# Optimization experiments

Hardware: AMD Instinct MI355X
Metric: run time of the kernel (lower is better)

Reference implementation:

```python
import jax, jax.numpy as jnp
import numpy as np

N_NODES = 20000
N_EDGES = 320000
H = 128
IN = 256  # num_hidden + num_in
SCALE = 30.0
EPS = 1e-5


def _ln(x, g, b):
    m = jnp.mean(x, axis=-1, keepdims=True)
    v = jnp.var(x, axis=-1, keepdims=True)
    return (x - m) * jax.lax.rsqrt(v + EPS) * g + b


def setup_inputs() -> dict:
    key = jax.random.key(0)
    ks = jax.random.split(key, 16)
    s_in = 1.0 / np.sqrt(IN)
    s_h = 1.0 / np.sqrt(H)
    s_4h = 1.0 / np.sqrt(4 * H)
    return {
        "h_V": jax.random.normal(ks[0], (N_NODES, H), jnp.float32),
        "h_E": jax.random.normal(ks[1], (N_EDGES, IN), jnp.float32),
        "edge_idx": jax.random.randint(ks[2], (2, N_EDGES), 0, N_NODES, jnp.int32),
        # weights stored (in, out): y = x @ W + b (equivalent to torch Linear)
        "W1_w": jax.random.uniform(ks[3], (IN, H), jnp.float32, -s_in, s_in),
        "W1_b": jax.random.uniform(ks[4], (H,), jnp.float32, -s_in, s_in),
        "W2_w": jax.random.uniform(ks[5], (H, H), jnp.float32, -s_h, s_h),
        "W2_b": jax.random.uniform(ks[6], (H,), jnp.float32, -s_h, s_h),
        "W3_w": jax.random.uniform(ks[7], (H, H), jnp.float32, -s_h, s_h),
        "W3_b": jax.random.uniform(ks[8], (H,), jnp.float32, -s_h, s_h),
        "n1_g": jnp.ones((H,), jnp.float32),
        "n1_b": jnp.zeros((H,), jnp.float32),
        "d1_w": jax.random.uniform(ks[9], (H, 4 * H), jnp.float32, -s_h, s_h),
        "d1_b": jax.random.uniform(ks[10], (4 * H,), jnp.float32, -s_h, s_h),
        "d2_w": jax.random.uniform(ks[11], (4 * H, H), jnp.float32, -s_4h, s_4h),
        "d2_b": jax.random.uniform(ks[12], (H,), jnp.float32, -s_4h, s_4h),
        "n2_g": jnp.ones((H,), jnp.float32),
        "n2_b": jnp.zeros((H,), jnp.float32),
    }


def reference(h_V, h_E, edge_idx, W1_w, W1_b, W2_w, W2_b, W3_w, W3_b,
              n1_g, n1_b, d1_w, d1_b, d2_w, d2_b, n2_g, n2_b):
    gelu = lambda x: jax.nn.gelu(x, approximate=False)  # torch F.gelu default = erf
    src_idx = edge_idx[0]
    # edge MLP: W3(gelu(W2(gelu(W1(h_E)))))
    h_message = gelu(h_E @ W1_w + W1_b)
    h_message = gelu(h_message @ W2_w + W2_b)
    h_message = h_message @ W3_w + W3_b
    # scatter_sum over source node, then scale
    dh = jax.ops.segment_sum(h_message, src_idx, num_segments=N_NODES) / SCALE
    h_V = _ln(h_V + dh, n1_g, n1_b)  # dropout is identity at eval
    dh = gelu(h_V @ d1_w + d1_b) @ d2_w + d2_b
    h_V = _ln(h_V + dh, n2_g, n2_b)
    return h_V
```

## Files before the change

### kernel.cpp

```cpp
#include <hip/hip_runtime.h>
#include <hip/hip_bf16.h>
#include <math.h>

#define NNODES 20000
#define NEDGES 320000
#define HDIM   128
#define INDIM  256
#define INV_SCALE (1.0f/30.0f)
#define LN_EPS 1e-5f

typedef __bf16 bf16x8 __attribute__((ext_vector_type(8)));
typedef float  f32x4  __attribute__((ext_vector_type(4)));
typedef _Float16 half4_t __attribute__((ext_vector_type(4)));
typedef _Float16 half8_t __attribute__((ext_vector_type(8)));
typedef unsigned short ushort_t;

__device__ __forceinline__ unsigned short f2bf(float f) {
    union { __hip_bfloat16 h; unsigned short u; } c;
    c.h = __float2bfloat16(f);
    return c.u;
}

__device__ __forceinline__ float gelu_fast(float x) {
    const float z = x * (1.595769122f + 0.071354816f * x * x);
    return x / (1.0f + __expf(-z));
}

__device__ __forceinline__ f32x4 mfma_bf16(bf16x8 a, bf16x8 b, f32x4 c) {
    return __builtin_amdgcn_mfma_f32_16x16x32_bf16(a, b, c, 0, 0, 0);
}

#define CVT8(dst, v0, v1) { union { bf16x8 v; ushort_t u[8]; } c_; \
    c_.u[0] = f2bf((v0).x); c_.u[1] = f2bf((v0).y); c_.u[2] = f2bf((v0).z); c_.u[3] = f2bf((v0).w); \
    c_.u[4] = f2bf((v1).x); c_.u[5] = f2bf((v1).y); c_.u[6] = f2bf((v1).z); c_.u[7] = f2bf((v1).w); \
    (dst) = c_.v; }

__global__ void prep_all(const float* __restrict__ W1, const float* __restrict__ W2,
                         const float* __restrict__ W3, ushort_t* __restrict__ WswE,
                         const float* __restrict__ D1, const float* __restrict__ D2,
                         ushort_t* __restrict__ D1sw, ushort_t* __restrict__ D2sw,
                         const int* __restrict__ src, int* __restrict__ cnt) {
    const int id = blockIdx.x * 256 + threadIdx.x;
    if (id < 65536) {
        const float* W; int base, idx; bool perm = false;
        if (id < 32768)      { W = W1; base = 0;     idx = id; }
        else if (id < 49152) { W = W2; base = 32768; idx = id - 32768; }
        else                 { W = W3; base = 49152; idx = id - 49152; perm = true; }
        const int j = idx & 7, lane = (idx >> 3) & 63, t = (idx >> 9) & 7, s = idx >> 12;
        const int k = s * 32 + (lane >> 4) * 8 + j;
        const int n = perm ? (2 * ((t >> 1) * 16 + (lane & 15)) + (t & 1))
                           : (t * 16 + (lane & 15));
        WswE[base + idx] = f2bf(W[k * HDIM + n]);
    } else if (id < 196608) {
        const int nid = id - 65536;
        if (nid < 65536) {
            const int idx = nid;
            const int j = idx & 7, lane = (idx >> 3) & 63, f = idx >> 9;
            const int t = f & 31, s = f >> 5;
            const int k = s * 32 + (lane >> 4) * 8 + j;
            const int n = t * 16 + (lane & 15);
            D1sw[idx] = f2bf(D1[k * 512 + n]);
        } else {
            const int idx = nid - 65536;
            const int j = idx & 7, lane = (idx >> 3) & 63, f = idx >> 9;
            const int t = f & 7, s = f >> 3;
            const int k = s * 32 + (lane >> 4) * 8 + j;
            const int n = t * 16 + (lane & 15);
            D2sw[idx] = f2bf(D2[k * HDIM + n]);
        }
    } else {
        const int e = id - 196608;
        if (e < NEDGES) atomicAdd(&cnt[src[e]], 1);
    }
}

__launch_bounds__(1024)
__global__ void scan_counts(const int* __restrict__ cnt,
                            int* __restrict__ off, int* __restrict__ off2) {
    __shared__ int tot[1024];
    const int t = threadIdx.x;
    const int base = t * 20;
    int local[20]; int s = 0;
    #pragma unroll
    for (int i = 0; i < 20; ++i) {
        const int v = (base + i < NNODES) ? cnt[base + i] : 0;
        local[i] = s; s += v;
    }
    tot[t] = s;
    __syncthreads();
    for (int d = 1; d < 1024; d <<= 1) {
        const int v = (t >= d) ? tot[t - d] : 0;
        __syncthreads();
        tot[t] += v;
        __syncthreads();
    }
    const int excl = (t == 0) ? 0 : tot[t - 1];
    #pragma unroll
    for (int i = 0; i < 20; ++i)
        if (base + i < NNODES) { off[base + i] = excl + local[i]; off2[base + i] = excl + local[i]; }
    if (t == 1023) off[NNODES] = NEDGES;
}

__global__ void fill_perm(const int* __restrict__ src, int* __restrict__ off2,
                          int* __restrict__ perm) {
    const int e = blockIdx.x * 256 + threadIdx.x;
    if (e < NEDGES) {
        const int p = atomicAdd(&off2[src[e]], 1);
        perm[p] = e;
    }
}

#define A1S 272
#define SY  136

__launch_bounds__(256, 3)
__global__ void edge_mlp_v2(const float* __restrict__ hE,
                            const ushort_t* __restrict__ Wsw,
                            const float* __restrict__ b1,
                            const float* __restrict__ b2,
                            const float* __restrict__ b3,
                            _Float16* __restrict__ msg) {
    __shared__ __align__(16) ushort_t A1[64 * A1S];
    __shared__ __align__(16) ushort_t A2[64 * SY];

    const int tid = threadIdx.x;
    const int wave = tid >> 6, lane = tid & 63;
    const int quad = lane >> 4, l16 = lane & 15;
    const size_t e0 = (size_t)blockIdx.x * 64;
    const int T0 = wave * 2;

    {
        const int row = tid >> 2, q = tid & 3;
        const float4* src = (const float4*)(hE + (e0 + row) * INDIM + q * 64);
        ushort_t* dst = A1 + row * A1S + q * 64;
        #pragma unroll
        for (int i = 0; i < 8; ++i) {
            const float4 v0 = src[2 * i], v1 = src[2 * i + 1];
            bf16x8 a; CVT8(a, v0, v1);
            *(bf16x8*)(dst + i * 8) = a;
        }
    }

    f32x4 acc[4][2];
    bf16x8 bcur[2], bnxt[2];

    #pragma unroll
    for (int t = 0; t < 2; ++t) {
        const float bv = b1[(T0 + t) * 16 + l16];
        #pragma unroll
        for (int rt = 0; rt < 4; ++rt) acc[rt][t] = (f32x4){bv, bv, bv, bv};
    }
    bcur[0] = *(const bf16x8*)(Wsw + (size_t)((0 * 8 + T0 + 0) * 64 + lane) * 8);
    bcur[1] = *(const bf16x8*)(Wsw + (size_t)((0 * 8 + T0 + 1) * 64 + lane) * 8);
    __syncthreads();
    #pragma unroll
    for (int s = 0; s < 8; ++s) {
        if (s < 7) {
            bnxt[0] = *(const bf16x8*)(Wsw + (size_t)(((s + 1) * 8 + T0 + 0) * 64 + lane) * 8);
            bnxt[1] = *(const bf16x8*)(Wsw + (size_t)(((s + 1) * 8 + T0 + 1) * 64 + lane) * 8);
        }
        bf16x8 a[4];
        #pragma unroll
        for (int rt = 0; rt < 4; ++rt)
            a[rt] = *(const bf16x8*)(A1 + (rt * 16 + l16) * A1S + s * 32 + quad * 8);
        #pragma unroll
        for (int rt = 0; rt < 4; ++rt) {
            acc[rt][0] = mfma_bf16(a[rt], bcur[0], acc[rt][0]);
            acc[rt][1] = mfma_bf16(a[rt], bcur[1], acc[rt][1]);
        }
        bcur[0] = bnxt[0]; bcur[1] = bnxt[1];
    }
    #pragma unroll
    for (int rt = 0; rt < 4; ++rt)
        #pragma unroll
        for (int t = 0; t < 2; ++t)
            #pragma unroll
            for (int r = 0; r < 4; ++r)
                A2[(rt * 16 + quad * 4 + r) * SY + (T0 + t) * 16 + l16] =
                    f2bf(gelu_fast(acc[rt][t][r]));
    __syncthreads();

    #pragma unroll
    for (int t = 0; t < 2; ++t) {
        const float bv = b2[(T0 + t) * 16 + l16];
        #pragma unroll
        for (int rt = 0; rt < 4; ++rt) acc[rt][t] = (f32x4){bv, bv, bv, bv};
    }
    bcur[0] = *(const bf16x8*)(Wsw + 32768 + (size_t)((0 * 8 + T0 + 0) * 64 + lane) * 8);
    bcur[1] = *(const bf16x8*)(Wsw + 32768 + (size_t)((0 * 8 + T0 + 1) * 64 + lane) * 8);
    #pragma unroll
    for (int s = 0; s < 4; ++s) {
        if (s < 3) {
            bnxt[0] = *(const bf16x8*)(Wsw + 32768 + (size_t)(((s + 1) * 8 + T0 + 0) * 64 + lane) * 8);
            bnxt[1] = *(const bf16x8*)(Wsw + 32768 + (size_t)(((s + 1) * 8 + T0 + 1) * 64 + lane) * 8);
        }
        bf16x8 a[4];
        #pragma unroll
        for (int rt = 0; rt < 4; ++rt)
            a[rt] = *(const bf16x8*)(A2 + (rt * 16 + l16) * SY + s * 32 + quad * 8);
        #pragma unroll
        for (int rt = 0; rt < 4; ++rt) {
            acc[rt][0] = mfma_bf16(a[rt], bcur[0], acc[rt][0]);
            acc[rt][1] = mfma_bf16(a[rt], bcur[1], acc[rt][1]);
        }
        bcur[0] = bnxt[0]; bcur[1] = bnxt[1];
    }
    __syncthreads();
    #pragma unroll
    for (int rt = 0; rt < 4; ++rt)
        #pragma unroll
        for (int t = 0; t < 2; ++t)
            #pragma unroll
            for (int r = 0; r < 4; ++r)
                A2[(rt * 16 + quad * 4 + r) * SY + (T0 + t) * 16 + l16] =
                    f2bf(gelu_fast(acc[rt][t][r]));
    __syncthreads();

    #pragma unroll
    for (int t = 0; t < 2; ++t) {
        const float bv = b3[2 * (wave * 16 + l16) + t];
        #pragma unroll
        for (int rt = 0; rt < 4; ++rt) acc[rt][t] = (f32x4){bv, bv, bv, bv};
    }
    bcur[0] = *(const bf16x8*)(Wsw + 49152 + (size_t)((0 * 8 + T0 + 0) * 64 + lane) * 8);
    bcur[1] = *(const bf16x8*)(Wsw + 49152 + (size_t)((0 * 8 + T0 + 1) * 64 + lane) * 8);
    #pragma unroll
    for (int s = 0; s < 4; ++s) {
        if (s < 3) {
            bnxt[0] = *(const bf16x8*)(Wsw + 49152 + (size_t)(((s + 1) * 8 + T0 + 0) * 64 + lane) * 8);
            bnxt[1] = *(const bf16x8*)(Wsw + 49152 + (size_t)(((s + 1) * 8 + T0 + 1) * 64 + lane) * 8);
        }
        bf16x8 a[4];
        #pragma unroll
        for (int rt = 0; rt < 4; ++rt)
            a[rt] = *(const bf16x8*)(A2 + (rt * 16 + l16) * SY + s * 32 + quad * 8);
        #pragma unroll
        for (int rt = 0; rt < 4; ++rt) {
            acc[rt][0] = mfma_bf16(a[rt], bcur[0], acc[rt][0]);
            acc[rt][1] = mfma_bf16(a[rt], bcur[1], acc[rt][1]);
        }
        bcur[0] = bnxt[0]; bcur[1] = bnxt[1];
    }

    #pragma unroll
    for (int rt = 0; rt < 4; ++rt)
        #pragma unroll
        for (int r = 0; r < 4; ++r) {
            const size_t row = e0 + rt * 16 + quad * 4 + r;
            union { _Float16 h[2]; unsigned int u; } pk;
            pk.h[0] = (_Float16)acc[rt][0][r];
            pk.h[1] = (_Float16)acc[rt][1][r];
            ((unsigned int*)(msg + row * HDIM))[wave * 16 + l16] = pk.u;
        }
}

__launch_bounds__(256)
__global__ void gather_sum(const _Float16* __restrict__ msg,
                           const int* __restrict__ perm,
                           const int* __restrict__ off,
                           const float* __restrict__ hV,
                           float* __restrict__ xout) {
    const int tid = threadIdx.x;
    const int slot = tid >> 5, l32 = tid & 31;
    const int node = blockIdx.x * 8 + slot;
    const int j0 = off[node], j1 = off[node + 1];
    float a0 = 0.f, a1 = 0.f, a2 = 0.f, a3 = 0.f;
    int j = j0;
    for (; j + 1 < j1; j += 2) {
        const int ea = perm[j], eb = perm[j + 1];
        const half4_t ma = *(const half4_t*)(msg + (size_t)ea * HDIM + l32 * 4);
        const half4_t mb = *(const half4_t*)(msg + (size_t)eb * HDIM + l32 * 4);
        a0 += (float)ma[0] + (float)mb[0];
        a1 += (float)ma[1] + (float)mb[1];
        a2 += (float)ma[2] + (float)mb[2];
        a3 += (float)ma[3] + (float)mb[3];
    }
    if (j < j1) {
        const int ea = perm[j];
        const half4_t ma = *(const half4_t*)(msg + (size_t)ea * HDIM + l32 * 4);
        a0 += (float)ma[0]; a1 += (float)ma[1]; a2 += (float)ma[2]; a3 += (float)ma[3];
    }
    const float4 hv = *(const float4*)(hV + (size_t)node * HDIM + l32 * 4);
    const float4 o = {hv.x + a0 * INV_SCALE, hv.y + a1 * INV_SCALE,
                      hv.z + a2 * INV_SCALE, hv.w + a3 * INV_SCALE};
    *(float4*)(xout + (size_t)node * HDIM + l32 * 4) = o;
}

__launch_bounds__(256)
__global__ void node_mfma_x(const float* __restrict__ xin,
                            const float* __restrict__ n1g, const float* __restrict__ n1b,
                            const ushort_t* __restrict__ D1sw, const float* __restrict__ D1b,
                            const ushort_t* __restrict__ D2sw, const float* __restrict__ D2b,
                            const float* __restrict__ n2g, const float* __restrict__ n2b,
                            float* __restrict__ out) {
    __shared__ __align__(16) float xs[32 * HDIM];
    __shared__ __align__(16) ushort_t h1a[32 * SY];
    __shared__ __align__(16) ushort_t ua[32 * 520];
    __shared__ float mu_s[32], rs_s[32];

    const int tid = threadIdx.x;
    const int wave = tid >> 6, lane = tid & 63;
    const int quad = lane >> 4, l16 = lane & 15;
    const int n0 = blockIdx.x * 32;

    #pragma unroll
    for (int it = 0; it < 4; ++it) {
        const int f4 = it * 256 + tid;
        ((float4*)xs)[f4] = ((const float4*)(xin + (size_t)n0 * HDIM))[f4];
    }
    __syncthreads();

    {
        const int row = tid >> 3, q = tid & 7;
        float s = 0.f, s2 = 0.f;
        #pragma unroll
        for (int c = 0; c < 16; ++c) { const float v = xs[row * HDIM + q * 16 + c]; s += v; s2 += v * v; }
        #pragma unroll
        for (int o = 1; o < 8; o <<= 1) { s += __shfl_xor(s, o); s2 += __shfl_xor(s2, o); }
        if (q == 0) {
            const float m = s * (1.0f / HDIM);
            mu_s[row] = m;
            rs_s[row] = rsqrtf(s2 * (1.0f / HDIM) - m * m + LN_EPS);
        }
    }
    __syncthreads();

    #pragma unroll
    for (int it = 0; it < 2; ++it) {
        const int g = it * 256 + tid;
        const int row = g >> 4, col = (g & 15) * 8;
        const float mu = mu_s[row], rs = rs_s[row];
        union { bf16x8 v; ushort_t u[8]; } c;
        #pragma unroll
        for (int jj = 0; jj < 8; ++jj) {
            const float h1 = (xs[row * HDIM + col + jj] - mu) * rs * n1g[col + jj] + n1b[col + jj];
            c.u[jj] = f2bf(h1);
        }
        *(bf16x8*)(h1a + row * SY + col) = c.v;
    }
    __syncthreads();

    {
        f32x4 acc1[2][8];
        #pragma unroll
        for (int t = 0; t < 8; ++t) {
            const float bv = D1b[wave * 128 + t * 16 + l16];
            acc1[0][t] = (f32x4){bv, bv, bv, bv};
            acc1[1][t] = acc1[0][t];
        }
        #pragma unroll
        for (int s = 0; s < 4; ++s) {
            bf16x8 a[2];
            #pragma unroll
            for (int rt = 0; rt < 2; ++rt)
                a[rt] = *(const bf16x8*)(h1a + (rt * 16 + l16) * SY + s * 32 + quad * 8);
            #pragma unroll
            for (int t = 0; t < 8; ++t) {
                const bf16x8 b = *(const bf16x8*)(D1sw + (size_t)((s * 32 + wave * 8 + t) * 64 + lane) * 8);
                acc1[0][t] = mfma_bf16(a[0], b, acc1[0][t]);
                acc1[1][t] = mfma_bf16(a[1], b, acc1[1][t]);
            }
        }
        #pragma unroll
        for (int rt = 0; rt < 2; ++rt)
            #pragma unroll
            for (int t = 0; t < 8; ++t)
                #pragma unroll
                for (int r = 0; r < 4; ++r)
                    ua[(rt * 16 + quad * 4 + r) * 520 + wave * 128 + t * 16 + l16] =
                        f2bf(gelu_fast(acc1[rt][t][r]));
    }
    __syncthreads();

    f32x4 acc2[2][2];
    acc2[0][0] = (f32x4){0,0,0,0}; acc2[0][1] = acc2[0][0];
    acc2[1][0] = acc2[0][0];       acc2[1][1] = acc2[0][0];
    #pragma unroll
    for (int s = 0; s < 16; ++s) {
        bf16x8 a[2];
        #pragma unroll
        for (int rt = 0; rt < 2; ++rt)
            a[rt] = *(const bf16x8*)(ua + (rt * 16 + l16) * 520 + s * 32 + quad * 8);
        #pragma unroll
        for (int tt = 0; tt < 2; ++tt) {
            const bf16x8 b = *(const bf16x8*)(D2sw + (size_t)((s * 8 + wave * 2 + tt) * 64 + lane) * 8);
            acc2[0][tt] = mfma_bf16(a[0], b, acc2[0][tt]);
            acc2[1][tt] = mfma_bf16(a[1], b, acc2[1][tt]);
        }
    }
    __syncthreads();

    float* yf = (float*)ua;
    #pragma unroll
    for (int rt = 0; rt < 2; ++rt)
        #pragma unroll
        for (int tt = 0; tt < 2; ++tt)
            #pragma unroll
            for (int r = 0; r < 4; ++r) {
                const int row = rt * 16 + quad * 4 + r;
                const int col = wave * 32 + tt * 16 + l16;
                const float h1 = (xs[row * HDIM + col] - mu_s[row]) * rs_s[row] * n1g[col] + n1b[col];
                yf[row * HDIM + col] = h1 + acc2[rt][tt][r] + D2b[col];
            }
    __syncthreads();

    {
        const int row = tid >> 3, q = tid & 7;
        float s = 0.f, s2 = 0.f;
        #pragma unroll
        for (int c = 0; c < 16; ++c) { const float v = yf[row * HDIM + q * 16 + c]; s += v; s2 += v * v; }
        #pragma unroll
        for (int o = 1; o < 8; o <<= 1) { s += __shfl_xor(s, o); s2 += __shfl_xor(s2, o); }
        if (q == 0) {
            const float m = s * (1.0f / HDIM);
            mu_s[row] = m;
            rs_s[row] = rsqrtf(s2 * (1.0f / HDIM) - m * m + LN_EPS);
        }
    }
    __syncthreads();

    #pragma unroll
    for (int it = 0; it < 4; ++it) {
        const int f4 = it * 256 + tid;
        const int row = f4 >> 5, col = (f4 & 31) * 4;
        const float4 y = ((const float4*)yf)[f4];
        const float mu = mu_s[row], rs = rs_s[row];
        float4 o;
        o.x = (y.x - mu) * rs * n2g[col + 0] + n2b[col + 0];
        o.y = (y.y - mu) * rs * n2g[col + 1] + n2b[col + 1];
        o.z = (y.z - mu) * rs * n2g[col + 2] + n2b[col + 2];
        o.w = (y.w - mu) * rs * n2g[col + 3] + n2b[col + 3];
        ((float4*)(out + (size_t)n0 * HDIM))[f4] = o;
    }
}

__launch_bounds__(256, 4)
__global__ void edge_mlp_mfma(const float* __restrict__ hE,
                              const int* __restrict__ edge_idx,
                              const ushort_t* __restrict__ Wsw,
                              const float* __restrict__ b1,
                              const float* __restrict__ b2,
                              const float* __restrict__ b3,
                              _Float16* __restrict__ dh) {
    __shared__ ushort_t A2[4][32 * SY];

    const int tid = threadIdx.x;
    const int wave = tid >> 6, lane = tid & 63;
    const int quad = lane >> 4, l16 = lane & 15;
    const size_t e0 = (size_t)blockIdx.x * 128 + wave * 32;
    ushort_t* Aw = A2[wave];

    f32x4 acc[2][8];

    #pragma unroll
    for (int t = 0; t < 8; ++t) {
        const float bv = b1[t * 16 + l16];
        acc[0][t] = (f32x4){bv, bv, bv, bv};
        acc[1][t] = acc[0][t];
    }
    #pragma unroll
    for (int s = 0; s < 8; ++s) {
        bf16x8 a[2];
        #pragma unroll
        for (int rt = 0; rt < 2; ++rt) {
            const float4* p = (const float4*)(hE + (e0 + rt * 16 + l16) * INDIM + s * 32 + quad * 8);
            const float4 v0 = p[0], v1 = p[1];
            bf16x8 av; CVT8(av, v0, v1);
            a[rt] = av;
        }
        #pragma unroll
        for (int t = 0; t < 8; ++t) {
            const bf16x8 b = *(const bf16x8*)(Wsw + (size_t)((s * 8 + t) * 64 + lane) * 8);
            acc[0][t] = mfma_bf16(a[0], b, acc[0][t]);
            acc[1][t] = mfma_bf16(a[1], b, acc[1][t]);
        }
    }
    #pragma unroll
    for (int rt = 0; rt < 2; ++rt)
        #pragma unroll
        for (int t = 0; t < 8; ++t)
            #pragma unroll
            for (int r = 0; r < 4; ++r)
                Aw[(rt * 16 + quad * 4 + r) * SY + t * 16 + l16] = f2bf(gelu_fast(acc[rt][t][r]));

    #pragma unroll
    for (int t = 0; t < 8; ++t) {
        const float bv = b2[t * 16 + l16];
        acc[0][t] = (f32x4){bv, bv, bv, bv};
        acc[1][t] = acc[0][t];
    }
    #pragma unroll
    for (int s = 0; s < 4; ++s) {
        bf16x8 a[2];
        #pragma unroll
        for (int rt = 0; rt < 2; ++rt)
            a[rt] = *(const bf16x8*)(Aw + (rt * 16 + l16) * SY + s * 32 + quad * 8);
        #pragma unroll
        for (int t = 0; t < 8; ++t) {
            const bf16x8 b = *(const bf16x8*)(Wsw + 32768 + (size_t)((s * 8 + t) * 64 + lane) * 8);
            acc[0][t] = mfma_bf16(a[0], b, acc[0][t]);
            acc[1][t] = mfma_bf16(a[1], b, acc[1][t]);
        }
    }
    #pragma unroll
    for (int rt = 0; rt < 2; ++rt)
        #pragma unroll
        for (int t = 0; t < 8; ++t)
            #pragma unroll
            for (int r = 0; r < 4; ++r)
                Aw[(rt * 16 + quad * 4 + r) * SY + t * 16 + l16] = f2bf(gelu_fast(acc[rt][t][r]));

    #pragma unroll
    for (int t = 0; t < 8; ++t) {
        const float bv = b3[2 * ((t >> 1) * 16 + l16) + (t & 1)];
        acc[0][t] = (f32x4){bv, bv, bv, bv};
        acc[1][t] = acc[0][t];
    }
    #pragma unroll
    for (int s = 0; s < 4; ++s) {
        bf16x8 a[2];
        #pragma unroll
        for (int rt = 0; rt < 2; ++rt)
            a[rt] = *(const bf16x8*)(Aw + (rt * 16 + l16) * SY + s * 32 + quad * 8);
        #pragma unroll
        for (int t = 0; t < 8; ++t) {
            const bf16x8 b = *(const bf16x8*)(Wsw + 49152 + (size_t)((s * 8 + t) * 64 + lane) * 8);
            acc[0][t] = mfma_bf16(a[0], b, acc[0][t]);
            acc[1][t] = mfma_bf16(a[1], b, acc[1][t]);
        }
    }

    #pragma unroll
    for (int rt = 0; rt < 2; ++rt)
        #pragma unroll
        for (int r = 0; r < 4; ++r) {
            const int e = (int)e0 + rt * 16 + quad * 4 + r;
            const int s = edge_idx[e];
            _Float16* dst = dh + (size_t)s * HDIM;
            #pragma unroll
            for (int u = 0; u < 4; ++u) {
                const int c = 2 * (u * 16 + l16);
                union { _Float16 h[2]; unsigned int u32; } pk;
                pk.h[0] = (_Float16)acc[rt][2 * u][r];
                pk.h[1] = (_Float16)acc[rt][2 * u + 1][r];
                asm volatile("global_atomic_pk_add_f16 %0, %1, off"
                             :: "v"(dst + c), "v"(pk.u32) : "memory");
            }
        }
}

__launch_bounds__(256)
__global__ void node_mfma(const float* __restrict__ hV, const _Float16* __restrict__ dh,
                          const float* __restrict__ n1g, const float* __restrict__ n1b,
                          const ushort_t* __restrict__ D1sw, const float* __restrict__ D1b,
                          const ushort_t* __restrict__ D2sw, const float* __restrict__ D2b,
                          const float* __restrict__ n2g, const float* __restrict__ n2b,
                          float* __restrict__ out) {
    __shared__ __align__(16) float xs[32 * HDIM];
    __shared__ __align__(16) ushort_t h1a[32 * SY];
    __shared__ __align__(16) ushort_t ua[32 * 520];
    __shared__ float mu_s[32], rs_s[32];

    const int tid = threadIdx.x;
    const int wave = tid >> 6, lane = tid & 63;
    const int quad = lane >> 4, l16 = lane & 15;
    const int n0 = blockIdx.x * 32;

    #pragma unroll
    for (int it = 0; it < 4; ++it) {
        const int f4 = it * 256 + tid;
        const float4 hv = ((const float4*)(hV + (size_t)n0 * HDIM))[f4];
        const half4_t dv = ((const half4_t*)(dh + (size_t)n0 * HDIM))[f4];
        ((float4*)xs)[f4] = (float4){hv.x + (float)dv[0] * INV_SCALE,
                                     hv.y + (float)dv[1] * INV_SCALE,
                                     hv.z + (float)dv[2] * INV_SCALE,
                                     hv.w + (float)dv[3] * INV_SCALE};
    }
    __syncthreads();

    {
        const int row = tid >> 3, q = tid & 7;
        float s = 0.f, s2 = 0.f;
        #pragma unroll
        for (int c = 0; c < 16; ++c) { const float v = xs[row * HDIM + q * 16 + c]; s += v; s2 += v * v; }
        #pragma unroll
        for (int o = 1; o < 8; o <<= 1) { s += __shfl_xor(s, o); s2 += __shfl_xor(s2, o); }
        if (q == 0) {
            const float m = s * (1.0f / HDIM);
            mu_s[row] = m;
            rs_s[row] = rsqrtf(s2 * (1.0f / HDIM) - m * m + LN_EPS);
        }
    }
    __syncthreads();

    #pragma unroll
    for (int it = 0; it < 2; ++it) {
        const int g = it * 256 + tid;
        const int row = g >> 4, col = (g & 15) * 8;
        const float mu = mu_s[row], rs = rs_s[row];
        union { bf16x8 v; ushort_t u[8]; } c;
        #pragma unroll
        for (int jj = 0; jj < 8; ++jj) {
            const float h1 = (xs[row * HDIM + col + jj] - mu) * rs * n1g[col + jj] + n1b[col + jj];
            c.u[jj] = f2bf(h1);
        }
        *(bf16x8*)(h1a + row * SY + col) = c.v;
    }
    __syncthreads();

    {
        f32x4 acc1[2][8];
        #pragma unroll
        for (int t = 0; t < 8; ++t) {
            const float bv = D1b[wave * 128 + t * 16 + l16];
            acc1[0][t] = (f32x4){bv, bv, bv, bv};
            acc1[1][t] = acc1[0][t];
        }
        #pragma unroll
        for (int s = 0; s < 4; ++s) {
            bf16x8 a[2];
            #pragma unroll
            for (int rt = 0; rt < 2; ++rt)
                a[rt] = *(const bf16x8*)(h1a + (rt * 16 + l16) * SY + s * 32 + quad * 8);
            #pragma unroll
            for (int t = 0; t < 8; ++t) {
                const bf16x8 b = *(const bf16x8*)(D1sw + (size_t)((s * 32 + wave * 8 + t) * 64 + lane) * 8);
                acc1[0][t] = mfma_bf16(a[0], b, acc1[0][t]);
                acc1[1][t] = mfma_bf16(a[1], b, acc1[1][t]);
            }
        }
        #pragma unroll
        for (int rt = 0; rt < 2; ++rt)
            #pragma unroll
            for (int t = 0; t < 8; ++t)
                #pragma unroll
                for (int r = 0; r < 4; ++r)
                    ua[(rt * 16 + quad * 4 + r) * 520 + wave * 128 + t * 16 + l16] =
                        f2bf(gelu_fast(acc1[rt][t][r]));
    }
    __syncthreads();

    f32x4 acc2[2][2];
    acc2[0][0] = (f32x4){0,0,0,0}; acc2[0][1] = acc2[0][0];
    acc2[1][0] = acc2[0][0];       acc2[1][1] = acc2[0][0];
    #pragma unroll
    for (int s = 0; s < 16; ++s) {
        bf16x8 a[2];
        #pragma unroll
        for (int rt = 0; rt < 2; ++rt)
            a[rt] = *(const bf16x8*)(ua + (rt * 16 + l16) * 520 + s * 32 + quad * 8);
        #pragma unroll
        for (int tt = 0; tt < 2; ++tt) {
            const bf16x8 b = *(const bf16x8*)(D2sw + (size_t)((s * 8 + wave * 2 + tt) * 64 + lane) * 8);
            acc2[0][tt] = mfma_bf16(a[0], b, acc2[0][tt]);
            acc2[1][tt] = mfma_bf16(a[1], b, acc2[1][tt]);
        }
    }
    __syncthreads();

    float* yf = (float*)ua;
    #pragma unroll
    for (int rt = 0; rt < 2; ++rt)
        #pragma unroll
        for (int tt = 0; tt < 2; ++tt)
            #pragma unroll
            for (int r = 0; r < 4; ++r) {
                const int row = rt * 16 + quad * 4 + r;
                const int col = wave * 32 + tt * 16 + l16;
                const float h1 = (xs[row * HDIM + col] - mu_s[row]) * rs_s[row] * n1g[col] + n1b[col];
                yf[row * HDIM + col] = h1 + acc2[rt][tt][r] + D2b[col];
            }
    __syncthreads();

    {
        const int row = tid >> 3, q = tid & 7;
        float s = 0.f, s2 = 0.f;
        #pragma unroll
        for (int c = 0; c < 16; ++c) { const float v = yf[row * HDIM + q * 16 + c]; s += v; s2 += v * v; }
        #pragma unroll
        for (int o = 1; o < 8; o <<= 1) { s += __shfl_xor(s, o); s2 += __shfl_xor(s2, o); }
        if (q == 0) {
            const float m = s * (1.0f / HDIM);
            mu_s[row] = m;
            rs_s[row] = rsqrtf(s2 * (1.0f / HDIM) - m * m + LN_EPS);
        }
    }
    __syncthreads();

    #pragma unroll
    for (int it = 0; it < 4; ++it) {
        const int f4 = it * 256 + tid;
        const int row = f4 >> 5, col = (f4 & 31) * 4;
        const float4 y = ((const float4*)yf)[f4];
        const float mu = mu_s[row], rs = rs_s[row];
        float4 o;
        o.x = (y.x - mu) * rs * n2g[col + 0] + n2b[col + 0];
        o.y = (y.y - mu) * rs * n2g[col + 1] + n2b[col + 1];
        o.z = (y.z - mu) * rs * n2g[col + 2] + n2b[col + 2];
        o.w = (y.w - mu) * rs * n2g[col + 3] + n2b[col + 3];
        ((float4*)(out + (size_t)n0 * HDIM))[f4] = o;
    }
}

#define NT 8
__device__ __forceinline__ void ln_stats32(const float* __restrict__ buf,
                                           float* __restrict__ mu_s,
                                           float* __restrict__ rs_s, int tid) {
    const int g = tid >> 5, lane = tid & 31;
    float s = 0.f, s2 = 0.f;
    #pragma unroll
    for (int c = lane; c < HDIM; c += 32) { const float v = buf[g * HDIM + c]; s += v; s2 += v * v; }
    #pragma unroll
    for (int o = 16; o; o >>= 1) { s += __shfl_xor(s, o, 32); s2 += __shfl_xor(s2, o, 32); }
    if (lane == 0) {
        const float m = s * (1.0f / HDIM);
        mu_s[g] = m;
        rs_s[g] = rsqrtf(s2 * (1.0f / HDIM) - m * m + LN_EPS);
    }
}

__launch_bounds__(256)
__global__ void node_update_f32(const float* __restrict__ hV, const _Float16* __restrict__ dh,
                                const float* __restrict__ n1g, const float* __restrict__ n1b,
                                const float* __restrict__ D1w, const float* __restrict__ D1b,
                                const float* __restrict__ D2w, const float* __restrict__ D2b,
                                const float* __restrict__ n2g, const float* __restrict__ n2b,
                                float* __restrict__ out) {
    __shared__ float h1s[NT * HDIM];
    __shared__ float us[NT * 512];
    __shared__ float vs[2 * NT * HDIM];
    __shared__ float mu_s[NT], rs_s[NT];
    const int tid = threadIdx.x;
    const int n0 = blockIdx.x * NT;
    for (int idx = tid; idx < NT * HDIM; idx += 256) {
        const int i = idx >> 7, c = idx & 127;
        const size_t g = (size_t)(n0 + i) * HDIM + c;
        h1s[idx] = hV[g] + (float)dh[g] * INV_SCALE;
    }
    __syncthreads();
    ln_stats32(h1s, mu_s, rs_s, tid);
    __syncthreads();
    for (int idx = tid; idx < NT * HDIM; idx += 256) {
        const int i = idx >> 7, c = idx & 127;
        h1s[idx] = (h1s[idx] - mu_s[i]) * rs_s[i] * n1g[c] + n1b[c];
    }
    __syncthreads();
    {
        const int o = 2 * tid;
        const float2 bv = *(const float2*)(D1b + o);
        float a0[NT], a1[NT];
        #pragma unroll
        for (int i = 0; i < NT; ++i) { a0[i] = bv.x; a1[i] = bv.y; }
        for (int k = 0; k < HDIM; ++k) {
            const float2 w = *(const float2*)(D1w + (size_t)k * 512 + o);
            #pragma unroll
            for (int i = 0; i < NT; ++i) {
                const float xv = h1s[i * HDIM + k];
                a0[i] += xv * w.x; a1[i] += xv * w.y;
            }
        }
        #pragma unroll
        for (int i = 0; i < NT; ++i) {
            us[i * 512 + o]     = gelu_fast(a0[i]);
            us[i * 512 + o + 1] = gelu_fast(a1[i]);
        }
    }
    __syncthreads();
    {
        const int o = tid & 127, half = tid >> 7;
        float a[NT];
        #pragma unroll
        for (int i = 0; i < NT; ++i) a[i] = 0.f;
        const int k0 = half * 256;
        for (int k = k0; k < k0 + 256; ++k) {
            const float w = D2w[(size_t)k * HDIM + o];
            #pragma unroll
            for (int i = 0; i < NT; ++i) a[i] += us[i * 512 + k] * w;
        }
        #pragma unroll
        for (int i = 0; i < NT; ++i) vs[(half * NT + i) * HDIM + o] = a[i];
    }
    __syncthreads();
    float* ys = us;
    for (int idx = tid; idx < NT * HDIM; idx += 256) {
        const int i = idx >> 7, c = idx & 127;
        ys[idx] = h1s[idx] + vs[i * HDIM + c] + vs[(NT + i) * HDIM + c] + D2b[c];
    }
    __syncthreads();
    ln_stats32(ys, mu_s, rs_s, tid);
    __syncthreads();
    for (int idx = tid; idx < NT * HDIM; idx += 256) {
        const int i = idx >> 7, c = idx & 127;
        out[(size_t)(n0 + i) * HDIM + c] = (ys[idx] - mu_s[i]) * rs_s[i] * n2g[c] + n2b[c];
    }
}

extern "C" void kernel_launch(void* const* d_in, const int* in_sizes, int n_in,
                              void* d_out, int out_size, void* d_ws, size_t ws_size,
                              hipStream_t stream) {
    const float* hV  = (const float*)d_in[0];
    const float* hE  = (const float*)d_in[1];
    const int*  eidx = (const int*)d_in[2];
    const float* W1w = (const float*)d_in[3];
    const float* W1b = (const float*)d_in[4];
    const float* W2w = (const float*)d_in[5];
    const float* W2b = (const float*)d_in[6];
    const float* W3w = (const float*)d_in[7];
    const float* W3b = (const float*)d_in[8];
    const float* n1g = (const float*)d_in[9];
    const float* n1b = (const float*)d_in[10];
    const float* D1w = (const float*)d_in[11];
    const float* D1b = (const float*)d_in[12];
    const float* D2w = (const float*)d_in[13];
    const float* D2b = (const float*)d_in[14];
    const float* n2g = (const float*)d_in[15];
    const float* n2b = (const float*)d_in[16];
    float* out = (float*)d_out;

    const size_t MSG_BYTES = (size_t)NEDGES * HDIM * sizeof(_Float16);
    const size_t EW_BYTES  = 65536 * 2;
    const size_t T1_BYTES  = MSG_BYTES + 3 * EW_BYTES
                           + (size_t)NEDGES * 4 + (size_t)NNODES * 4
                           + (size_t)(NNODES + 1) * 4 + (size_t)NNODES * 4;
    const size_t DH_BYTES  = (size_t)NNODES * HDIM * sizeof(_Float16);
    const size_t T2_BYTES  = DH_BYTES + 3 * EW_BYTES;

    if (ws_size >= T1_BYTES) {
        char* p = (char*)d_ws;
        _Float16* msg  = (_Float16*)p;            p += MSG_BYTES;
        ushort_t* WswE = (ushort_t*)p;            p += EW_BYTES;
        ushort_t* D1sw = (ushort_t*)p;            p += EW_BYTES;
        ushort_t* D2sw = (ushort_t*)p;            p += EW_BYTES;
        int* perm = (int*)p;                      p += (size_t)NEDGES * 4;
        int* cnt  = (int*)p;                      p += (size_t)NNODES * 4;
        int* off  = (int*)p;                      p += (size_t)(NNODES + 1) * 4;
        int* off2 = (int*)p;

        hipMemsetAsync(cnt, 0, (size_t)NNODES * 4, stream);
        prep_all<<<2019, 256, 0, stream>>>(W1w, W2w, W3w, WswE, D1w, D2w, D1sw, D2sw, eidx, cnt);
        scan_counts<<<1, 1024, 0, stream>>>(cnt, off, off2);
        fill_perm<<<(NEDGES + 255) / 256, 256, 0, stream>>>(eidx, off2, perm);
        edge_mlp_v2<<<NEDGES / 64, 256, 0, stream>>>(hE, WswE, W1b, W2b, W3b, msg);
        gather_sum<<<NNODES / 8, 256, 0, stream>>>(msg, perm, off, hV, out);
        node_mfma_x<<<NNODES / 32, 256, 0, stream>>>(out, n1g, n1b,
                                                     D1sw, D1b, D2sw, D2b, n2g, n2b, out);
    } else if (ws_size >= T2_BYTES) {
        _Float16* dh = (_Float16*)d_ws;
        ushort_t* WswE = (ushort_t*)((char*)d_ws + DH_BYTES);
        ushort_t* D1sw = (ushort_t*)((char*)d_ws + DH_BYTES + EW_BYTES);
        ushort_t* D2sw = (ushort_t*)((char*)d_ws + DH_BYTES + 2 * EW_BYTES);
        hipMemsetAsync(dh, 0, DH_BYTES, stream);
        prep_all<<<2019, 256, 0, stream>>>(W1w, W2w, W3w, WswE, D1w, D2w, D1sw, D2sw, eidx, (int*)WswE );
        edge_mlp_mfma<<<NEDGES / 128, 256, 0, stream>>>(hE, eidx, WswE, W1b, W2b, W3b, dh);
        node_mfma<<<NNODES / 32, 256, 0, stream>>>(hV, dh, n1g, n1b, D1sw, D1b, D2sw, D2b, n2g, n2b, out);
    } else {
        _Float16* dh = (_Float16*)d_ws;
        ushort_t* WswE = (ushort_t*)((char*)d_out + (size_t)out_size * 4 - EW_BYTES);
        hipMemsetAsync(dh, 0, DH_BYTES, stream);
        prep_all<<<2019, 256, 0, stream>>>(W1w, W2w, W3w, WswE, D1w, D2w,
                                            (ushort_t*)dh, (ushort_t*)dh,
                                           eidx, (int*)dh);
        hipMemsetAsync(dh, 0, DH_BYTES, stream);
        edge_mlp_mfma<<<NEDGES / 128, 256, 0, stream>>>(hE, eidx, WswE, W1b, W2b, W3b, dh);
        node_update_f32<<<NNODES / NT, 256, 0, stream>>>(hV, dh, n1g, n1b, D1w, D1b, D2w, D2b, n2g, n2b, out);
    }
}
```

Before: 627.8 us.

## Halve edge-MLP input LDS buffer, stage second K-half via registers, raise occupancy

The first edge-MLP layer now stages only half of the 256-wide bf16 input tile in shared memory at a time. The second half is prefetched into registers while the first four K-steps run, then written over the same buffer. This cuts LDS per block so launch bounds can ask for 4 blocks per CU instead of 3, trading two extra barriers and more registers for more occupancy and load/compute overlap. Fallback paths also skip unneeded prep work via null pointers and drop a redundant memset.

```diff
diff --git a/kernel.cpp b/kernel.cpp
--- a/kernel.cpp
+++ b/kernel.cpp
@@ -52,6 +52,7 @@
                            : (t * 16 + (lane & 15));
         WswE[base + idx] = f2bf(W[k * HDIM + n]);
     } else if (id < 196608) {
+        if (!D1sw) return;
         const int nid = id - 65536;
         if (nid < 65536) {
             const int idx = nid;
@@ -69,6 +70,7 @@
             D2sw[idx] = f2bf(D2[k * HDIM + n]);
         }
     } else {
+        if (!cnt) return;
         const int e = id - 196608;
         if (e < NEDGES) atomicAdd(&cnt[src[e]], 1);
     }
@@ -110,17 +112,17 @@
     }
 }
 
-#define A1S 272
+#define A1H 136
 #define SY  136
 
-__launch_bounds__(256, 3)
-__global__ void edge_mlp_v2(const float* __restrict__ hE,
+__launch_bounds__(256, 4)
+__global__ void edge_mlp_v3(const float* __restrict__ hE,
                             const ushort_t* __restrict__ Wsw,
                             const float* __restrict__ b1,
                             const float* __restrict__ b2,
                             const float* __restrict__ b3,
                             _Float16* __restrict__ msg) {
-    __shared__ __align__(16) ushort_t A1[64 * A1S];
+    __shared__ __align__(16) ushort_t A1h[64 * A1H];
     __shared__ __align__(16) ushort_t A2[64 * SY];
 
     const int tid = threadIdx.x;
@@ -129,17 +131,20 @@
     const size_t e0 = (size_t)blockIdx.x * 64;
     const int T0 = wave * 2;
 
-    {
-        const int row = tid >> 2, q = tid & 3;
-        const float4* src = (const float4*)(hE + (e0 + row) * INDIM + q * 64);
-        ushort_t* dst = A1 + row * A1S + q * 64;
-        #pragma unroll
-        for (int i = 0; i < 8; ++i) {
-            const float4 v0 = src[2 * i], v1 = src[2 * i + 1];
-            bf16x8 a; CVT8(a, v0, v1);
-            *(bf16x8*)(dst + i * 8) = a;
-        }
-    }
+    const int srow = tid >> 2, sq = tid & 3;
+    const float4* sp = (const float4*)(hE + (e0 + srow) * INDIM) + sq * 8;
+    ushort_t* sd = A1h + srow * A1H + sq * 32;
+
+    float4 rg[8];
+    #pragma unroll
+    for (int i = 0; i < 8; ++i) rg[i] = sp[i];
+    #pragma unroll
+    for (int i = 0; i < 4; ++i) {
+        bf16x8 v; CVT8(v, rg[2 * i], rg[2 * i + 1]);
+        *(bf16x8*)(sd + i * 8) = v;
+    }
+    #pragma unroll
+    for (int i = 0; i < 8; ++i) rg[i] = sp[32 + i];
 
     f32x4 acc[4][2];
     bf16x8 bcur[2], bnxt[2];
@@ -150,11 +155,36 @@
         #pragma unroll
         for (int rt = 0; rt < 4; ++rt) acc[rt][t] = (f32x4){bv, bv, bv, bv};
     }
-    bcur[0] = *(const bf16x8*)(Wsw + (size_t)((0 * 8 + T0 + 0) * 64 + lane) * 8);
-    bcur[1] = *(const bf16x8*)(Wsw + (size_t)((0 * 8 + T0 + 1) * 64 + lane) * 8);
-    __syncthreads();
-    #pragma unroll
-    for (int s = 0; s < 8; ++s) {
+    bcur[0] = *(const bf16x8*)(Wsw + (size_t)((T0 + 0) * 64 + lane) * 8);
+    bcur[1] = *(const bf16x8*)(Wsw + (size_t)((T0 + 1) * 64 + lane) * 8);
+    __syncthreads();
+
+    #pragma unroll
+    for (int s = 0; s < 4; ++s) {
+        bnxt[0] = *(const bf16x8*)(Wsw + (size_t)(((s + 1) * 8 + T0 + 0) * 64 + lane) * 8);
+        bnxt[1] = *(const bf16x8*)(Wsw + (size_t)(((s + 1) * 8 + T0 + 1) * 64 + lane) * 8);
+        bf16x8 a[4];
+        #pragma unroll
+        for (int rt = 0; rt < 4; ++rt)
+            a[rt] = *(const bf16x8*)(A1h + (rt * 16 + l16) * A1H + s * 32 + quad * 8);
+        #pragma unroll
+        for (int rt = 0; rt < 4; ++rt) {
+            acc[rt][0] = mfma_bf16(a[rt], bcur[0], acc[rt][0]);
+            acc[rt][1] = mfma_bf16(a[rt], bcur[1], acc[rt][1]);
+        }
+        bcur[0] = bnxt[0]; bcur[1] = bnxt[1];
+    }
+    __syncthreads();
+
+    #pragma unroll
+    for (int i = 0; i < 4; ++i) {
+        bf16x8 v; CVT8(v, rg[2 * i], rg[2 * i + 1]);
+        *(bf16x8*)(sd + i * 8) = v;
+    }
+    __syncthreads();
+
+    #pragma unroll
+    for (int s = 4; s < 8; ++s) {
         if (s < 7) {
             bnxt[0] = *(const bf16x8*)(Wsw + (size_t)(((s + 1) * 8 + T0 + 0) * 64 + lane) * 8);
             bnxt[1] = *(const bf16x8*)(Wsw + (size_t)(((s + 1) * 8 + T0 + 1) * 64 + lane) * 8);
@@ -162,7 +192,7 @@
         bf16x8 a[4];
         #pragma unroll
         for (int rt = 0; rt < 4; ++rt)
-            a[rt] = *(const bf16x8*)(A1 + (rt * 16 + l16) * A1S + s * 32 + quad * 8);
+            a[rt] = *(const bf16x8*)(A1h + (rt * 16 + l16) * A1H + (s - 4) * 32 + quad * 8);
         #pragma unroll
         for (int rt = 0; rt < 4; ++rt) {
             acc[rt][0] = mfma_bf16(a[rt], bcur[0], acc[rt][0]);
@@ -186,8 +216,8 @@
         #pragma unroll
         for (int rt = 0; rt < 4; ++rt) acc[rt][t] = (f32x4){bv, bv, bv, bv};
     }
-    bcur[0] = *(const bf16x8*)(Wsw + 32768 + (size_t)((0 * 8 + T0 + 0) * 64 + lane) * 8);
-    bcur[1] = *(const bf16x8*)(Wsw + 32768 + (size_t)((0 * 8 + T0 + 1) * 64 + lane) * 8);
+    bcur[0] = *(const bf16x8*)(Wsw + 32768 + (size_t)((T0 + 0) * 64 + lane) * 8);
+    bcur[1] = *(const bf16x8*)(Wsw + 32768 + (size_t)((T0 + 1) * 64 + lane) * 8);
     #pragma unroll
     for (int s = 0; s < 4; ++s) {
         if (s < 3) {
@@ -222,8 +252,8 @@
         #pragma unroll
         for (int rt = 0; rt < 4; ++rt) acc[rt][t] = (f32x4){bv, bv, bv, bv};
     }
-    bcur[0] = *(const bf16x8*)(Wsw + 49152 + (size_t)((0 * 8 + T0 + 0) * 64 + lane) * 8);
-    bcur[1] = *(const bf16x8*)(Wsw + 49152 + (size_t)((0 * 8 + T0 + 1) * 64 + lane) * 8);
+    bcur[0] = *(const bf16x8*)(Wsw + 49152 + (size_t)((T0 + 0) * 64 + lane) * 8);
+    bcur[1] = *(const bf16x8*)(Wsw + 49152 + (size_t)((T0 + 1) * 64 + lane) * 8);
     #pragma unroll
     for (int s = 0; s < 4; ++s) {
         if (s < 3) {
@@ -840,7 +870,7 @@
         prep_all<<<2019, 256, 0, stream>>>(W1w, W2w, W3w, WswE, D1w, D2w, D1sw, D2sw, eidx, cnt);
         scan_counts<<<1, 1024, 0, stream>>>(cnt, off, off2);
         fill_perm<<<(NEDGES + 255) / 256, 256, 0, stream>>>(eidx, off2, perm);
-        edge_mlp_v2<<<NEDGES / 64, 256, 0, stream>>>(hE, WswE, W1b, W2b, W3b, msg);
+        edge_mlp_v3<<<NEDGES / 64, 256, 0, stream>>>(hE, WswE, W1b, W2b, W3b, msg);
         gather_sum<<<NNODES / 8, 256, 0, stream>>>(msg, perm, off, hV, out);
         node_mfma_x<<<NNODES / 32, 256, 0, stream>>>(out, n1g, n1b,
                                                      D1sw, D1b, D2sw, D2b, n2g, n2b, out);
@@ -850,17 +880,16 @@
         ushort_t* D1sw = (ushort_t*)((char*)d_ws + DH_BYTES + EW_BYTES);
         ushort_t* D2sw = (ushort_t*)((char*)d_ws + DH_BYTES + 2 * EW_BYTES);
         hipMemsetAsync(dh, 0, DH_BYTES, stream);
-        prep_all<<<2019, 256, 0, stream>>>(W1w, W2w, W3w, WswE, D1w, D2w, D1sw, D2sw, eidx, (int*)WswE );
+        prep_all<<<2019, 256, 0, stream>>>(W1w, W2w, W3w, WswE, D1w, D2w, D1sw, D2sw,
+                                           eidx, nullptr);
         edge_mlp_mfma<<<NEDGES / 128, 256, 0, stream>>>(hE, eidx, WswE, W1b, W2b, W3b, dh);
         node_mfma<<<NNODES / 32, 256, 0, stream>>>(hV, dh, n1g, n1b, D1sw, D1b, D2sw, D2b, n2g, n2b, out);
     } else {
         _Float16* dh = (_Float16*)d_ws;
         ushort_t* WswE = (ushort_t*)((char*)d_out + (size_t)out_size * 4 - EW_BYTES);
         hipMemsetAsync(dh, 0, DH_BYTES, stream);
-        prep_all<<<2019, 256, 0, stream>>>(W1w, W2w, W3w, WswE, D1w, D2w,
-                                            (ushort_t*)dh, (ushort_t*)dh,
-                                           eidx, (int*)dh);
-        hipMemsetAsync(dh, 0, DH_BYTES, stream);
+        prep_all<<<2019, 256, 0, stream>>>(W1w, W2w, W3w, WswE, D1w, D2w, nullptr, nullptr,
+                                           eidx, nullptr);
         edge_mlp_mfma<<<NEDGES / 128, 256, 0, stream>>>(hE, eidx, WswE, W1b, W2b, W3b, dh);
         node_update_f32<<<NNODES / NT, 256, 0, stream>>>(hV, dh, n1g, n1b, D1w, D1b, D2w, D2b, n2g, n2b, out);
     }
```

Measured after the change: 615.4 us. 1.02x faster.
